# Kernel optimization log

Measured on AMD Instinct MI355X. Metric: run time of the kernel, lower is better.

## Reference

```python
import jax, jax.numpy as jnp
import numpy as np

CP = (96, 96, 96)      # control-point grid size (D, H, W)
NSTEPS = 7             # VecInt int_steps
N_TP = 4               # timepoints
# all ordered pairs i<j: tid 'ti_to_tj' -> ref=i, flo=j  (K = 6)
REF_IDX = np.array([0, 0, 0, 1, 1, 2])
FLO_IDX = np.array([1, 2, 3, 2, 3, 3])


def _make_grid(shape):
    axes = [jnp.arange(s, dtype=jnp.float32) for s in shape]
    return jnp.stack(jnp.meshgrid(*axes, indexing='ij'), axis=0)  # (3, D, H, W)

GRID = _make_grid(CP)


def trilinear_sample(vol, coords):
    """Sample channels-first volume at absolute voxel coordinates.

    vol:    (C, D, H, W) field values
    coords: (3, D, H, W) absolute (i, j, k) voxel coordinates
    returns (C, D, H, W); border (clamp) handling at edges.
    """
    D, H, W = vol.shape[1:]
    x, y, z = coords[0], coords[1], coords[2]
    x0f = jnp.floor(x); y0f = jnp.floor(y); z0f = jnp.floor(z)
    fx = x - x0f; fy = y - y0f; fz = z - z0f
    x0 = jnp.clip(x0f.astype(jnp.int32), 0, D - 1)
    x1 = jnp.clip(x0 + 1, 0, D - 1)
    y0 = jnp.clip(y0f.astype(jnp.int32), 0, H - 1)
    y1 = jnp.clip(y0 + 1, 0, H - 1)
    z0 = jnp.clip(z0f.astype(jnp.int32), 0, W - 1)
    z1 = jnp.clip(z0 + 1, 0, W - 1)

    c000 = vol[:, x0, y0, z0]; c001 = vol[:, x0, y0, z1]
    c010 = vol[:, x0, y1, z0]; c011 = vol[:, x0, y1, z1]
    c100 = vol[:, x1, y0, z0]; c101 = vol[:, x1, y0, z1]
    c110 = vol[:, x1, y1, z0]; c111 = vol[:, x1, y1, z1]

    c00 = c000 * (1 - fz) + c001 * fz
    c01 = c010 * (1 - fz) + c011 * fz
    c10 = c100 * (1 - fz) + c101 * fz
    c11 = c110 * (1 - fz) + c111 * fz
    c0 = c00 * (1 - fy) + c01 * fy
    c1 = c10 * (1 - fy) + c11 * fy
    return c0 * (1 - fx) + c1 * fx


def vecint(v):
    """Scaling-and-squaring integration of stationary velocity field v: (3,D,H,W)."""
    v = v * (1.0 / 2.0 ** NSTEPS)
    for _ in range(NSTEPS):
        v = v + trilinear_sample(v, GRID + v)
    return v


def compose_fields(f1, f2):
    """(grid + f1 + f2(grid + f1)) - grid, fields (3,D,H,W)."""
    return f1 + trilinear_sample(f2, GRID + f1)


def setup_inputs() -> dict:
    key = jax.random.key(0)
    k1, k2 = jax.random.split(key)
    T = jax.random.normal(k1, (N_TP, 3) + CP, dtype=jnp.float32)
    R = jax.random.normal(k2, CP + (3, len(REF_IDX)), dtype=jnp.float32)
    return {"T": T, "R": R}


def reference(T, R):
    # integrate +/- velocity for every timepoint once (same math as per-pair calls)
    F_pos = jax.vmap(vecint)(T)           # (N, 3, D, H, W) = integrate(T[t])
    F_neg = jax.vmap(vecint)(-T)          # (N, 3, D, H, W) = integrate(-T[t])
    ref = jnp.asarray(REF_IDX)
    flo = jnp.asarray(FLO_IDX)
    # R_hat[k] = compose(integrate(-T[ref_k]), integrate(T[flo_k]))  -> (K,3,D,H,W)
    R_hat = jax.vmap(compose_fields)(F_neg[ref], F_pos[flo])
    # original permutes R_hat to (D,H,W,3,K); equivalently permute R the other way
    residue = R_hat - jnp.transpose(R, (4, 3, 0, 1, 2))  # (K,3,D,H,W)
    # l1 cost: sum_k,x sqrt(sum_c residue^2)
    loss = jnp.sum(jnp.sqrt(jnp.sum(residue ** 2, axis=1)))
    return loss
```

## Files before the change

### kernel.cpp

```cpp
#include <hip/hip_runtime.h>
#include <hip/hip_fp16.h>

#define NV    884736
#define NB    3456
#define DIM   96
#define DIM2  9216
#define NF    6
#define SLACK 32


union H4 { uint2 u; __half2 h2[2]; };
union H8 { uint4 u; __half2 h2[4]; };

struct F3 { float x, y, z; };

__device__ __forceinline__ F3 lerp3(F3 a, F3 b, float t, float omt) {
    F3 r;
    r.x = a.x * omt + b.x * t;
    r.y = a.y * omt + b.y * t;
    r.z = a.z * omt + b.z * t;
    return r;
}

__device__ __forceinline__ uint2 pack_h4(float x, float y, float z) {
    H4 v;
    v.h2[0] = __floats2half2_rn(x, y);
    v.h2[1] = __floats2half2_rn(z, 0.0f);
    return v.u;
}

__device__ __forceinline__ F3 unpack_h4(uint2 raw) {
    H4 v; v.u = raw;
    float2 xy = __half22float2(v.h2[0]);
    float2 zp = __half22float2(v.h2[1]);
    F3 r; r.x = xy.x; r.y = xy.y; r.z = zp.x;
    return r;
}

struct TriIdx { int idx[4]; float fx, fy, fz; };

__device__ __forceinline__ TriIdx tri_prep(float x, float y, float z) {
    TriIdx t;
    float xf = floorf(x), yf = floorf(y), zf = floorf(z);
    t.fx = x - xf; t.fy = y - yf;
    float fz = z - zf;
    int x0 = (int)xf; x0 = x0 < 0 ? 0 : (x0 > DIM - 1 ? DIM - 1 : x0);
    int y0 = (int)yf; y0 = y0 < 0 ? 0 : (y0 > DIM - 1 ? DIM - 1 : y0);
    int z0 = (int)zf; z0 = z0 < 0 ? 0 : (z0 > DIM - 1 ? DIM - 1 : z0);
    int x1 = x0 + 1; if (x1 > DIM - 1) x1 = DIM - 1;
    int y1 = y0 + 1; if (y1 > DIM - 1) y1 = DIM - 1;
    t.fz = (z0 < DIM - 1) ? fz : 0.0f;
    int X0 = x0 * DIM2, X1 = x1 * DIM2;
    int Y0 = y0 * DIM,  Y1 = y1 * DIM;
    t.idx[0] = X0 + Y0 + z0;
    t.idx[1] = X0 + Y1 + z0;
    t.idx[2] = X1 + Y0 + z0;
    t.idx[3] = X1 + Y1 + z0;
    return t;
}

__device__ __forceinline__ void tri_gather(const uint2* __restrict__ f,
                                           const TriIdx& t, H8 c[4]) {
    #pragma unroll
    for (int q = 0; q < 4; q++)
        c[q].u = *(const uint4*)(f + t.idx[q]);
}

__device__ __forceinline__ F3 tri_combine(const TriIdx& t, const H8 c[4]) {
    float gz = 1.0f - t.fz, gy = 1.0f - t.fy, gx = 1.0f - t.fx;
    F3 pz[4];
    #pragma unroll
    for (int q = 0; q < 4; q++) {
        float2 xy0 = __half22float2(c[q].h2[0]);
        float2 z0p = __half22float2(c[q].h2[1]);
        float2 xy1 = __half22float2(c[q].h2[2]);
        float2 z1p = __half22float2(c[q].h2[3]);
        F3 lo; lo.x = xy0.x; lo.y = xy0.y; lo.z = z0p.x;
        F3 hi; hi.x = xy1.x; hi.y = xy1.y; hi.z = z1p.x;
        pz[q] = lerp3(lo, hi, t.fz, gz);
    }
    F3 c0 = lerp3(pz[0], pz[1], t.fy, gy);
    F3 c1 = lerp3(pz[2], pz[3], t.fy, gy);
    return lerp3(c0, c1, t.fx, gx);
}

__global__ __launch_bounds__(256) void init_kernel(const float* __restrict__ T,
                                                   uint2* __restrict__ bufA,
                                                   uint2* __restrict__ bufB,
                                                   float* __restrict__ out) {
    int t = blockIdx.y;
    int l = blockIdx.x * 256 + threadIdx.x;
    if (t == 0 && l == 0) out[0] = 0.0f;
    if (t == 0 && l < SLACK) {
        bufA[(size_t)NF * NV + l] = make_uint2(0u, 0u);
        bufB[(size_t)NF * NV + l] = make_uint2(0u, 0u);
    }
    const float inv = 1.0f / 128.0f;
    float vx = T[(size_t)(t * 3 + 0) * NV + l] * inv;
    float vy = T[(size_t)(t * 3 + 1) * NV + l] * inv;
    float vz = T[(size_t)(t * 3 + 2) * NV + l] * inv;
    if (t >= 1) bufA[(size_t)(t - 1) * NV + l] = pack_h4( vx,  vy,  vz);
    if (t <= 2) bufA[(size_t)(t + 3) * NV + l] = pack_h4(-vx, -vy, -vz);
}

#define STEP_VB   NB
#define STEP_W    (STEP_VB * NF)
#define STEP_CHK  (STEP_W / 8)
__global__ __launch_bounds__(256) void step_kernel(const uint2* __restrict__ src,
                                                   uint2* __restrict__ dst) {
    int b   = blockIdx.x;
    int w   = (b & 7) * STEP_CHK + (b >> 3);
    int f   = w / STEP_VB;
    int vb  = w - f * STEP_VB;
    const uint2* __restrict__ s = src + (size_t)f * NV;
    uint2*       __restrict__ d = dst + (size_t)f * NV;

    int l   = vb * 256 + threadIdx.x;
    int i   = l / DIM2;
    int rem = l - i * DIM2;
    int j   = rem / DIM;
    int k   = rem - j * DIM;

    F3 v = unpack_h4(s[l]);
    TriIdx t = tri_prep((float)i + v.x, (float)j + v.y, (float)k + v.z);
    H8 c[4];
    tri_gather(s, t, c);
    F3 smp = tri_combine(t, c);
    d[l] = pack_h4(v.x + smp.x, v.y + smp.y, v.z + smp.z);
}

__global__ __launch_bounds__(256) void loss_kernel(const uint2* __restrict__ fields,
                                                   const float* __restrict__ R,
                                                   float* __restrict__ out) {
    int b = blockIdx.x;
    int vb = (b & 7) * (NB / 8) + (b >> 3);
    int l = vb * 256 + threadIdx.x;
    int k = l % DIM;
    int j = (l / DIM) % DIM;
    int i = l / DIM2;
    float fi = (float)i, fj = (float)j, fk = (float)k;

    F3 f1c[3];
    #pragma unroll
    for (int r = 0; r < 3; r++)
        f1c[r] = unpack_h4(fields[(size_t)(3 + r) * NV + l]);

    float rbuf[18];
    const float* Rl = R + (size_t)l * 18;
    #pragma unroll
    for (int q = 0; q < 18; q++) rbuf[q] = Rl[q];

    const int REFI[6] = {0, 0, 0, 1, 1, 2};
    const int FLOF[6] = {0, 1, 2, 1, 2, 2};

    float acc = 0.0f;
    #pragma unroll
    for (int p = 0; p < 6; p += 2) {
        F3 f1a = f1c[REFI[p]];
        F3 f1b = f1c[REFI[p + 1]];
        const uint2* __restrict__ f2a = fields + (size_t)FLOF[p]     * NV;
        const uint2* __restrict__ f2b = fields + (size_t)FLOF[p + 1] * NV;
        TriIdx ta = tri_prep(fi + f1a.x, fj + f1a.y, fk + f1a.z);
        TriIdx tb = tri_prep(fi + f1b.x, fj + f1b.y, fk + f1b.z);
        H8 ca[4], cb[4];
        tri_gather(f2a, ta, ca);
        tri_gather(f2b, tb, cb);
        F3 sa = tri_combine(ta, ca);
        F3 sb = tri_combine(tb, cb);
        float rx = f1a.x + sa.x - rbuf[0 * 6 + p];
        float ry = f1a.y + sa.y - rbuf[1 * 6 + p];
        float rz = f1a.z + sa.z - rbuf[2 * 6 + p];
        acc += sqrtf(rx * rx + ry * ry + rz * rz);
        rx = f1b.x + sb.x - rbuf[0 * 6 + p + 1];
        ry = f1b.y + sb.y - rbuf[1 * 6 + p + 1];
        rz = f1b.z + sb.z - rbuf[2 * 6 + p + 1];
        acc += sqrtf(rx * rx + ry * ry + rz * rz);
    }

    __shared__ float wsum[4];
    int lane = threadIdx.x & 63;
    int wid  = threadIdx.x >> 6;
    #pragma unroll
    for (int off = 32; off > 0; off >>= 1)
        acc += __shfl_down(acc, off, 64);
    if (lane == 0) wsum[wid] = acc;
    __syncthreads();
    if (threadIdx.x == 0) {
        float s = wsum[0] + wsum[1] + wsum[2] + wsum[3];
        atomicAdd(out, s);
    }
}

extern "C" void kernel_launch(void* const* d_in, const int* in_sizes, int n_in,
                              void* d_out, int out_size, void* d_ws, size_t ws_size,
                              hipStream_t stream) {
    const float* T = (const float*)d_in[0];
    const float* R = (const float*)d_in[1];
    float* out = (float*)d_out;

    uint2* bufA = (uint2*)d_ws;
    uint2* bufB = bufA + (size_t)NF * NV + SLACK;

    dim3 blk(256);
    init_kernel<<<dim3(NB, 4), blk, 0, stream>>>(T, bufA, bufB, out);

    uint2* src = bufA;
    uint2* dst = bufB;
    for (int s = 0; s < 7; s++) {
        step_kernel<<<STEP_W, blk, 0, stream>>>(src, dst);
        uint2* tmp = src; src = dst; dst = tmp;
    }
    loss_kernel<<<NB, blk, 0, stream>>>(src, R, out);
}
```

Measured before the change: 348.0 us.

## Fuse init and integration steps into one cooperative persistent kernel with grid sync

```diff
diff --git a/kernel.cpp b/kernel.cpp
--- a/kernel.cpp
+++ b/kernel.cpp
@@ -1,12 +1,21 @@
 #include <hip/hip_runtime.h>
 #include <hip/hip_fp16.h>
+#include <hip/hip_cooperative_groups.h>
+
+namespace cg = cooperative_groups;
 
 #define NV    884736
 #define NB    3456
 #define DIM   96
 #define DIM2  9216
 #define NF    6
+#define NSTEPS 7
 #define SLACK 32
+
+#define STEP_W  (NB * NF)
+#define GRID_I  864
+#define UPB     24
+#define XCHK    (STEP_W / 8)
 
 
 union H4 { uint2 u; __half2 h2[2]; };
@@ -84,98 +93,106 @@
     return lerp3(c0, c1, t.fx, gx);
 }
 
-__global__ __launch_bounds__(256) void init_kernel(const float* __restrict__ T,
-                                                   uint2* __restrict__ bufA,
-                                                   uint2* __restrict__ bufB,
-                                                   float* __restrict__ out) {
-    int t = blockIdx.y;
-    int l = blockIdx.x * 256 + threadIdx.x;
-    if (t == 0 && l == 0) out[0] = 0.0f;
-    if (t == 0 && l < SLACK) {
-        bufA[(size_t)NF * NV + l] = make_uint2(0u, 0u);
-        bufB[(size_t)NF * NV + l] = make_uint2(0u, 0u);
+__global__ __launch_bounds__(256, 4) void integrate_kernel(const float* __restrict__ T,
+                                                           uint2* __restrict__ bufA,
+                                                           uint2* __restrict__ bufB,
+                                                           float* __restrict__ out) {
+    cg::grid_group grid = cg::this_grid();
+    const int tid = threadIdx.x;
+    const int b   = blockIdx.x;
+    const int w0  = (b & 7) * XCHK + (b >> 3) * UPB;
+
+    if (b == 0 && tid == 0) out[0] = 0.0f;
+    if (b == 0 && tid < SLACK) {
+        bufA[(size_t)NF * NV + tid] = make_uint2(0u, 0u);
+        bufB[(size_t)NF * NV + tid] = make_uint2(0u, 0u);
     }
     const float inv = 1.0f / 128.0f;
-    float vx = T[(size_t)(t * 3 + 0) * NV + l] * inv;
-    float vy = T[(size_t)(t * 3 + 1) * NV + l] * inv;
-    float vz = T[(size_t)(t * 3 + 2) * NV + l] * inv;
-    if (t >= 1) bufA[(size_t)(t - 1) * NV + l] = pack_h4( vx,  vy,  vz);
-    if (t <= 2) bufA[(size_t)(t + 3) * NV + l] = pack_h4(-vx, -vy, -vz);
-}
-
-#define STEP_VB   NB
-#define STEP_W    (STEP_VB * NF)
-#define STEP_CHK  (STEP_W / 8)
-__global__ __launch_bounds__(256) void step_kernel(const uint2* __restrict__ src,
-                                                   uint2* __restrict__ dst) {
-    int b   = blockIdx.x;
-    int w   = (b & 7) * STEP_CHK + (b >> 3);
-    int f   = w / STEP_VB;
-    int vb  = w - f * STEP_VB;
-    const uint2* __restrict__ s = src + (size_t)f * NV;
-    uint2*       __restrict__ d = dst + (size_t)f * NV;
-
-    int l   = vb * 256 + threadIdx.x;
-    int i   = l / DIM2;
-    int rem = l - i * DIM2;
-    int j   = rem / DIM;
-    int k   = rem - j * DIM;
-
-    F3 v = unpack_h4(s[l]);
-    TriIdx t = tri_prep((float)i + v.x, (float)j + v.y, (float)k + v.z);
-    H8 c[4];
-    tri_gather(s, t, c);
-    F3 smp = tri_combine(t, c);
-    d[l] = pack_h4(v.x + smp.x, v.y + smp.y, v.z + smp.z);
-}
-
+    #pragma unroll 2
+    for (int u = 0; u < UPB; u++) {
+        int w  = w0 + u;
+        int f  = w / NB;
+        int vb = w - f * NB;
+        int l  = vb * 256 + tid;
+        int tr = (f < 3) ? (f + 1) : (f - 3);
+        float sg = (f < 3) ? inv : -inv;
+        float vx = T[(size_t)(tr * 3 + 0) * NV + l] * sg;
+        float vy = T[(size_t)(tr * 3 + 1) * NV + l] * sg;
+        float vz = T[(size_t)(tr * 3 + 2) * NV + l] * sg;
+        bufA[(size_t)f * NV + l] = pack_h4(vx, vy, vz);
+    }
+    grid.sync();
+
+    uint2* src = bufA;
+    uint2* dst = bufB;
+    for (int s = 0; s < NSTEPS; s++) {
+        #pragma unroll 2
+        for (int u = 0; u < UPB; u++) {
+            int w  = w0 + u;
+            int f  = w / NB;
+            int vb = w - f * NB;
+            int l  = vb * 256 + tid;
+            const uint2* __restrict__ sp = src + (size_t)f * NV;
+            int i   = l / DIM2;
+            int rem = l - i * DIM2;
+            int j   = rem / DIM;
+            int k   = rem - j * DIM;
+            F3 v = unpack_h4(sp[l]);
+            TriIdx tt = tri_prep((float)i + v.x, (float)j + v.y, (float)k + v.z);
+            H8 c[4];
+            tri_gather(sp, tt, c);
+            F3 smp = tri_combine(tt, c);
+            dst[(size_t)f * NV + l] = pack_h4(v.x + smp.x, v.y + smp.y, v.z + smp.z);
+        }
+        grid.sync();
+        uint2* tmp = src; src = dst; dst = tmp;
+    }
+}
+
+#define NBL3 (NB * 3)
+#define LCHK (NBL3 / 8)
 __global__ __launch_bounds__(256) void loss_kernel(const uint2* __restrict__ fields,
                                                    const float* __restrict__ R,
                                                    float* __restrict__ out) {
-    int b = blockIdx.x;
-    int vb = (b & 7) * (NB / 8) + (b >> 3);
-    int l = vb * 256 + threadIdx.x;
+    int b  = blockIdx.x;
+    int wl = (b & 7) * LCHK + (b >> 3);
+    int pp = wl / NB;
+    int vb = wl - pp * NB;
+    int l  = vb * 256 + threadIdx.x;
     int k = l % DIM;
     int j = (l / DIM) % DIM;
     int i = l / DIM2;
     float fi = (float)i, fj = (float)j, fk = (float)k;
 
-    F3 f1c[3];
-    #pragma unroll
-    for (int r = 0; r < 3; r++)
-        f1c[r] = unpack_h4(fields[(size_t)(3 + r) * NV + l]);
-
-    float rbuf[18];
+    int p0 = pp * 2, p1 = p0 + 1;
+    int refa = pp >> 1, refb = pp;
+    int floa = pp ? 2 : 0, flob = 1 + (pp >> 1);
+
     const float* Rl = R + (size_t)l * 18;
-    #pragma unroll
-    for (int q = 0; q < 18; q++) rbuf[q] = Rl[q];
-
-    const int REFI[6] = {0, 0, 0, 1, 1, 2};
-    const int FLOF[6] = {0, 1, 2, 1, 2, 2};
-
-    float acc = 0.0f;
-    #pragma unroll
-    for (int p = 0; p < 6; p += 2) {
-        F3 f1a = f1c[REFI[p]];
-        F3 f1b = f1c[REFI[p + 1]];
-        const uint2* __restrict__ f2a = fields + (size_t)FLOF[p]     * NV;
-        const uint2* __restrict__ f2b = fields + (size_t)FLOF[p + 1] * NV;
-        TriIdx ta = tri_prep(fi + f1a.x, fj + f1a.y, fk + f1a.z);
-        TriIdx tb = tri_prep(fi + f1b.x, fj + f1b.y, fk + f1b.z);
-        H8 ca[4], cb[4];
-        tri_gather(f2a, ta, ca);
-        tri_gather(f2b, tb, cb);
-        F3 sa = tri_combine(ta, ca);
-        F3 sb = tri_combine(tb, cb);
-        float rx = f1a.x + sa.x - rbuf[0 * 6 + p];
-        float ry = f1a.y + sa.y - rbuf[1 * 6 + p];
-        float rz = f1a.z + sa.z - rbuf[2 * 6 + p];
-        acc += sqrtf(rx * rx + ry * ry + rz * rz);
-        rx = f1b.x + sb.x - rbuf[0 * 6 + p + 1];
-        ry = f1b.y + sb.y - rbuf[1 * 6 + p + 1];
-        rz = f1b.z + sb.z - rbuf[2 * 6 + p + 1];
-        acc += sqrtf(rx * rx + ry * ry + rz * rz);
-    }
+    float ra_x = Rl[0 * 6 + p0], ra_y = Rl[1 * 6 + p0], ra_z = Rl[2 * 6 + p0];
+    float rb_x = Rl[0 * 6 + p1], rb_y = Rl[1 * 6 + p1], rb_z = Rl[2 * 6 + p1];
+
+    F3 f1a = unpack_h4(fields[(size_t)(3 + refa) * NV + l]);
+    F3 f1b = unpack_h4(fields[(size_t)(3 + refb) * NV + l]);
+    const uint2* __restrict__ f2a = fields + (size_t)floa * NV;
+    const uint2* __restrict__ f2b = fields + (size_t)flob * NV;
+
+    TriIdx ta = tri_prep(fi + f1a.x, fj + f1a.y, fk + f1a.z);
+    TriIdx tb = tri_prep(fi + f1b.x, fj + f1b.y, fk + f1b.z);
+    H8 ca[4], cb[4];
+    tri_gather(f2a, ta, ca);
+    tri_gather(f2b, tb, cb);
+    F3 sa = tri_combine(ta, ca);
+    F3 sb = tri_combine(tb, cb);
+
+    float rx = f1a.x + sa.x - ra_x;
+    float ry = f1a.y + sa.y - ra_y;
+    float rz = f1a.z + sa.z - ra_z;
+    float acc = sqrtf(rx * rx + ry * ry + rz * rz);
+    rx = f1b.x + sb.x - rb_x;
+    ry = f1b.y + sb.y - rb_y;
+    rz = f1b.z + sb.z - rb_z;
+    acc += sqrtf(rx * rx + ry * ry + rz * rz);
 
     __shared__ float wsum[4];
     int lane = threadIdx.x & 63;
@@ -201,14 +218,9 @@
     uint2* bufA = (uint2*)d_ws;
     uint2* bufB = bufA + (size_t)NF * NV + SLACK;
 
-    dim3 blk(256);
-    init_kernel<<<dim3(NB, 4), blk, 0, stream>>>(T, bufA, bufB, out);
-
-    uint2* src = bufA;
-    uint2* dst = bufB;
-    for (int s = 0; s < 7; s++) {
-        step_kernel<<<STEP_W, blk, 0, stream>>>(src, dst);
-        uint2* tmp = src; src = dst; dst = tmp;
-    }
-    loss_kernel<<<NB, blk, 0, stream>>>(src, R, out);
-}
+    void* args[] = { (void*)&T, (void*)&bufA, (void*)&bufB, (void*)&out };
+    hipLaunchCooperativeKernel((const void*)integrate_kernel,
+                               dim3(GRID_I), dim3(256), args, 0, stream);
+
+    loss_kernel<<<NBL3, dim3(256), 0, stream>>>(bufB, R, out);
+}
```

Result: slower. 1.361 ms (+291.0%).

## Stage neighbouring rows in shared memory for early scaling-squaring steps

Applied to the files above, without the earlier changes.

```diff
diff --git a/kernel.cpp b/kernel.cpp
--- a/kernel.cpp
+++ b/kernel.cpp
@@ -106,6 +106,7 @@
 #define STEP_VB   NB
 #define STEP_W    (STEP_VB * NF)
 #define STEP_CHK  (STEP_W / 8)
+
 __global__ __launch_bounds__(256) void step_kernel(const uint2* __restrict__ src,
                                                    uint2* __restrict__ dst) {
     int b   = blockIdx.x;
@@ -127,6 +128,100 @@
     tri_gather(s, t, c);
     F3 smp = tri_combine(t, c);
     d[l] = pack_h4(v.x + smp.x, v.y + smp.y, v.z + smp.z);
+}
+
+#define TROWS     18
+#define ROWB      784
+#define TILE_B    (TROWS * ROWB)
+#define TCHUNKS   (TROWS * 48)
+__global__ __launch_bounds__(256) void step_tiled_kernel(const uint2* __restrict__ src,
+                                                         uint2* __restrict__ dst) {
+    __shared__ __align__(16) unsigned char tile[TILE_B];
+    int tid = threadIdx.x;
+    int b   = blockIdx.x;
+    int w   = (b & 7) * STEP_CHK + (b >> 3);
+    int f   = w / STEP_VB;
+    int vb  = w - f * STEP_VB;
+    const uint2* __restrict__ s = src + (size_t)f * NV;
+    uint2*       __restrict__ d = dst + (size_t)f * NV;
+
+    int l0   = vb * 256;
+    int i    = l0 / DIM2;
+    int rem0 = l0 - i * DIM2;
+    int jb   = rem0 / DIM;
+
+    #pragma unroll
+    for (int rnd = 0; rnd < 4; rnd++) {
+        int c = rnd * 256 + tid;
+        if (c < TCHUNKS) {
+            int r   = c / 48;
+            int col = c - r * 48;
+            int p   = r / 6;
+            int rr  = r - p * 6;
+            int ic  = i - 1 + p;  ic = ic < 0 ? 0 : (ic > DIM - 1 ? DIM - 1 : ic);
+            int jc  = jb - 1 + rr; jc = jc < 0 ? 0 : (jc > DIM - 1 ? DIM - 1 : jc);
+            uint4 val = *(const uint4*)(s + ic * DIM2 + jc * DIM + col * 2);
+            *(uint4*)(tile + r * ROWB + col * 16) = val;
+        }
+    }
+    if (tid < TROWS)
+        *(uint4*)(tile + tid * ROWB + 768) = make_uint4(0u, 0u, 0u, 0u);
+    __syncthreads();
+
+    int remt = rem0 + tid;
+    int j = remt / DIM;
+    int k = remt - j * DIM;
+
+    F3 v = unpack_h4(*(const uint2*)(tile + (6 + (j - jb + 1)) * ROWB + k * 8));
+
+    float x = (float)i + v.x, y = (float)j + v.y, z = (float)k + v.z;
+    float xf = floorf(x), yf = floorf(y), zf = floorf(z);
+    TriIdx t;
+    t.fx = x - xf; t.fy = y - yf;
+    float fzr = z - zf;
+    int x0 = (int)xf; x0 = x0 < 0 ? 0 : (x0 > DIM - 1 ? DIM - 1 : x0);
+    int y0 = (int)yf; y0 = y0 < 0 ? 0 : (y0 > DIM - 1 ? DIM - 1 : y0);
+    int z0 = (int)zf; z0 = z0 < 0 ? 0 : (z0 > DIM - 1 ? DIM - 1 : z0);
+    t.fz = (z0 < DIM - 1) ? fzr : 0.0f;
+
+    unsigned ux = (unsigned)(x0 - (i - 1));
+    unsigned uy = (unsigned)(y0 - (j - 1));
+    unsigned uz = (unsigned)(z0 - (k - 1));
+    bool in_tile = (ux <= 1u) & (uy <= 1u) & (uz <= 1u);
+
+    H8 c[4];
+    if (in_tile) {
+        int b00 = ((x0 - (i - 1)) * 6 + (y0 - (jb - 1))) * ROWB + z0 * 8;
+        c[0].h2[0] = ((const __half2*)(tile + b00))[0];
+        c[0].h2[1] = ((const __half2*)(tile + b00))[1];
+        c[0].h2[2] = ((const __half2*)(tile + b00 + 8))[0];
+        c[0].h2[3] = ((const __half2*)(tile + b00 + 8))[1];
+        int b01 = b00 + ROWB;
+        c[1].h2[0] = ((const __half2*)(tile + b01))[0];
+        c[1].h2[1] = ((const __half2*)(tile + b01))[1];
+        c[1].h2[2] = ((const __half2*)(tile + b01 + 8))[0];
+        c[1].h2[3] = ((const __half2*)(tile + b01 + 8))[1];
+        int b10 = b00 + 6 * ROWB;
+        c[2].h2[0] = ((const __half2*)(tile + b10))[0];
+        c[2].h2[1] = ((const __half2*)(tile + b10))[1];
+        c[2].h2[2] = ((const __half2*)(tile + b10 + 8))[0];
+        c[2].h2[3] = ((const __half2*)(tile + b10 + 8))[1];
+        int b11 = b10 + ROWB;
+        c[3].h2[0] = ((const __half2*)(tile + b11))[0];
+        c[3].h2[1] = ((const __half2*)(tile + b11))[1];
+        c[3].h2[2] = ((const __half2*)(tile + b11 + 8))[0];
+        c[3].h2[3] = ((const __half2*)(tile + b11 + 8))[1];
+    } else {
+        int x1 = x0 + 1; if (x1 > DIM - 1) x1 = DIM - 1;
+        int y1 = y0 + 1; if (y1 > DIM - 1) y1 = DIM - 1;
+        t.idx[0] = x0 * DIM2 + y0 * DIM + z0;
+        t.idx[1] = x0 * DIM2 + y1 * DIM + z0;
+        t.idx[2] = x1 * DIM2 + y0 * DIM + z0;
+        t.idx[3] = x1 * DIM2 + y1 * DIM + z0;
+        tri_gather(s, t, c);
+    }
+    F3 smp = tri_combine(t, c);
+    d[l0 + tid] = pack_h4(v.x + smp.x, v.y + smp.y, v.z + smp.z);
 }
 
 __global__ __launch_bounds__(256) void loss_kernel(const uint2* __restrict__ fields,
@@ -207,7 +302,10 @@
     uint2* src = bufA;
     uint2* dst = bufB;
     for (int s = 0; s < 7; s++) {
-        step_kernel<<<STEP_W, blk, 0, stream>>>(src, dst);
+        if (s < 6)
+            step_tiled_kernel<<<STEP_W, blk, 0, stream>>>(src, dst);
+        else
+            step_kernel<<<STEP_W, blk, 0, stream>>>(src, dst);
         uint2* tmp = src; src = dst; dst = tmp;
     }
     loss_kernel<<<NB, blk, 0, stream>>>(src, R, out);
```

New measurement: 384.0 us. 1.1x slower.
